# Kernel tuning notes

Measured on AMD Instinct MI355X. Metric: run time of the kernel, lower is better.

## Reference

```python
import jax, jax.numpy as jnp
import numpy as np

N = 10000        # num nodes
E = 160000       # num edges
C = 128          # hidden_channels
SCALE = 0.0625   # scale_factor = 1/avg_degree
EPS = 1.1920929e-07  # torch RMSNorm default eps = finfo(float32).eps


def setup_inputs() -> dict:
    key = jax.random.key(0)
    ks = jax.random.split(key, 10)
    s = jax.random.normal(ks[0], (N, 1, C), dtype=jnp.float32)
    v = jax.random.normal(ks[1], (N, 3, C), dtype=jnp.float32)
    edge_index = jax.random.randint(ks[2], (2, E), 0, N, dtype=jnp.int64)
    rbf_filter = jax.random.normal(ks[3], (E, 1, 3 * C), dtype=jnp.float32)
    edge_vector = jax.random.normal(ks[4], (E, 3), dtype=jnp.float32)
    # phi MLP params (Linear(C,C) -> SiLU -> Dropout(eval) -> Linear(C,3C))
    w1 = jax.random.normal(ks[5], (C, C), dtype=jnp.float32) / np.sqrt(C)
    b1 = jnp.zeros((C,), dtype=jnp.float32)
    w2 = jax.random.normal(ks[6], (3 * C, C), dtype=jnp.float32) / np.sqrt(C)
    b2 = jnp.zeros((3 * C,), dtype=jnp.float32)
    rms_w = jnp.ones((C,), dtype=jnp.float32)  # RMSNorm elementwise affine weight
    return {"s": s, "v": v, "edge_index": edge_index, "rbf_filter": rbf_filter,
            "edge_vector": edge_vector, "w1": w1, "b1": b1, "w2": w2, "b2": b2,
            "rms_w": rms_w}


def reference(s, v, edge_index, rbf_filter, edge_vector, w1, b1, w2, b2, rms_w):
    i, j = edge_index[0], edge_index[1]
    # RMSNorm over last dim
    s_norm = s * jax.lax.rsqrt(jnp.mean(s * s, axis=-1, keepdims=True) + EPS) * rms_w
    # phi MLP (dropout is identity in eval mode)
    h = jax.nn.silu(jnp.einsum('nkc,dc->nkd', s_norm, w1) + b1)
    phi_s = jnp.einsum('nkc,dc->nkd', h, w2) + b2          # [N,1,3C]
    filt = phi_s[j] * rbf_filter                           # [E,1,3C]
    m_s, m_vv, m_vs = jnp.split(filt, 3, axis=-1)          # each [E,1,C]
    ds = jax.ops.segment_sum(m_s, i, num_segments=N)       # [N,1,C]
    gate = v[j] * m_vv + edge_vector[:, :, None] * m_vs    # [E,3,C]
    dv = jax.ops.segment_sum(gate, i, num_segments=N)      # [N,3,C]
    s_out = s + ds * SCALE
    v_out = v + dv * SCALE
    return s_out, v_out
```

## Files before the change

kernel.cpp:

```cpp
#include <hip/hip_runtime.h>
#include <hip/hip_fp16.h>
#include <math.h>

#define NN 10000
#define NE 160000
#define CH 128
#define SCALE_F 0.0625f
#define EPS_F 1.1920929e-07f

__device__ __forceinline__ unsigned short f2bf(float x) {
    unsigned int u = __float_as_uint(x);
    u += 0x7FFFu + ((u >> 16) & 1u);
    return (unsigned short)(u >> 16);
}
__device__ __forceinline__ unsigned int pack2bf(float a, float b) {
    return (unsigned int)f2bf(a) | ((unsigned int)f2bf(b) << 16);
}
__device__ __forceinline__ float bf_lo(unsigned int u) { return __uint_as_float(u << 16); }
__device__ __forceinline__ float bf_hi(unsigned int u) { return __uint_as_float(u & 0xFFFF0000u); }
__device__ __forceinline__ float4 bfq(uint2 u) {
    return make_float4(bf_lo(u.x), bf_hi(u.x), bf_lo(u.y), bf_hi(u.y));
}

__global__ __launch_bounds__(256) void detect_zero_kernel(const int* __restrict__ ei,
                                                          int* __restrict__ flag,
                                                          int* __restrict__ counts) {
    int t = blockIdx.x * 256 + threadIdx.x;
    if (t < NN) counts[t] = 0;
    if (blockIdx.x == 0 && threadIdx.x < 64) {
        int val = ei[2 * threadIdx.x + 1];
        unsigned long long b = __ballot(val != 0);
        if (threadIdx.x == 0) *flag = (b == 0ULL) ? 1 : 0;
    }
}

__global__ __launch_bounds__(256) void count_kernel(const int* __restrict__ ei,
                                                    const int* __restrict__ flag,
                                                    int* __restrict__ counts) {
    int e = blockIdx.x * 256 + threadIdx.x;
    if (e >= NE) return;
    int i = (*flag) ? ei[2 * (size_t)e] : ei[e];
    atomicAdd(&counts[i], 1);
}

__global__ __launch_bounds__(1024) void scan_kernel(const int* __restrict__ counts,
                                                    int* __restrict__ offsets,
                                                    int* __restrict__ cursor) {
    __shared__ int sm[1024];
    const int t = threadIdx.x;
    const int base = t * 10;
    int vals[10];
    int lsum = 0;
    #pragma unroll
    for (int k = 0; k < 10; ++k) {
        int idx = base + k;
        int v = (idx < NN) ? counts[idx] : 0;
        vals[k] = v;
        lsum += v;
    }
    sm[t] = lsum;
    __syncthreads();
    #pragma unroll
    for (int off = 1; off < 1024; off <<= 1) {
        int add = (t >= off) ? sm[t - off] : 0;
        __syncthreads();
        sm[t] += add;
        __syncthreads();
    }
    int run = sm[t] - lsum;
    #pragma unroll
    for (int k = 0; k < 10; ++k) {
        int idx = base + k;
        if (idx < NN) { offsets[idx] = run; cursor[idx] = run; }
        run += vals[k];
    }
}

__global__ __launch_bounds__(256) void bucket_kernel(const int* __restrict__ ei,
                                                     const int* __restrict__ flag,
                                                     const float* __restrict__ ev,
                                                     int* __restrict__ cursor,
                                                     int4* __restrict__ bucket) {
    int e = blockIdx.x * 256 + threadIdx.x;
    if (e >= NE) return;
    int i, j;
    if (*flag) {
        i = ei[2 * (size_t)e];
        j = ei[2 * ((size_t)NE + e)];
    } else {
        i = ei[e];
        j = ei[NE + e];
    }
    float e0 = ev[(size_t)e * 3 + 0];
    float e1 = ev[(size_t)e * 3 + 1];
    float e2 = ev[(size_t)e * 3 + 2];
    __half2 h01 = __floats2half2_rn(e0, e1);
    __half  h2v = __float2half_rn(e2);
    unsigned int u01 = *reinterpret_cast<unsigned int*>(&h01);
    unsigned int u2  = (unsigned int)(*reinterpret_cast<unsigned short*>(&h2v));
    int pos = atomicAdd(&cursor[i], 1);
    bucket[pos] = make_int4(e, j, (int)u01, (int)u2);
}

__global__ __launch_bounds__(256) void phi_kernel(const float* __restrict__ s,
                                                  const float* __restrict__ v,
                                                  const float* __restrict__ w1,
                                                  const float* __restrict__ b1,
                                                  const float* __restrict__ w2,
                                                  const float* __restrict__ b2,
                                                  const float* __restrict__ rms_w,
                                                  unsigned int* __restrict__ rec) {
    __shared__ float sn[8][132];
    __shared__ float hh[8][132];

    const int t = threadIdx.x;
    const int n0 = blockIdx.x * 8;

    {
        const int m = t >> 5;
        const int l = t & 31;
        const int n = n0 + m;
        const float2* vsrc = (const float2*)(v + (size_t)n * 384);
        unsigned int* vdst = rec + (size_t)n * 384 + 192;
        #pragma unroll
        for (int k = 0; k < 6; ++k) {
            float2 a = vsrc[k * 32 + l];
            vdst[k * 32 + l] = pack2bf(a.x, a.y);
        }
    }

    {
        const int m = t >> 5;
        const int l = t & 31;
        const int n = n0 + m;
        float4 sv = ((const float4*)(s + (size_t)n * CH))[l];
        float ss = sv.x * sv.x + sv.y * sv.y + sv.z * sv.z + sv.w * sv.w;
        #pragma unroll
        for (int off = 16; off > 0; off >>= 1) ss += __shfl_xor(ss, off, 32);
        const float sc = rsqrtf(ss * (1.0f / CH) + EPS_F);
        float4 rw = ((const float4*)rms_w)[l];
        float4* dst = (float4*)&sn[m][l * 4];
        float4 o;
        o.x = sv.x * sc * rw.x;
        o.y = sv.y * sc * rw.y;
        o.z = sv.z * sc * rw.z;
        o.w = sv.w * sc * rw.w;
        *dst = o;
    }
    __syncthreads();

    const int d  = t & 127;
    const int mh = (t >> 7) * 4;

    {
        float acc0, acc1, acc2, acc3;
        const float bb = b1[d];
        acc0 = acc1 = acc2 = acc3 = bb;
        const float4* w1v = (const float4*)(w1 + (size_t)d * CH);
        #pragma unroll 4
        for (int kc = 0; kc < 32; ++kc) {
            float4 w = w1v[kc];
            float4 s0 = *(const float4*)&sn[mh + 0][kc * 4];
            float4 s1 = *(const float4*)&sn[mh + 1][kc * 4];
            float4 s2 = *(const float4*)&sn[mh + 2][kc * 4];
            float4 s3 = *(const float4*)&sn[mh + 3][kc * 4];
            acc0 += w.x * s0.x + w.y * s0.y + w.z * s0.z + w.w * s0.w;
            acc1 += w.x * s1.x + w.y * s1.y + w.z * s1.z + w.w * s1.w;
            acc2 += w.x * s2.x + w.y * s2.y + w.z * s2.z + w.w * s2.w;
            acc3 += w.x * s3.x + w.y * s3.y + w.z * s3.z + w.w * s3.w;
        }
        hh[mh + 0][d] = acc0 / (1.0f + __expf(-acc0));
        hh[mh + 1][d] = acc1 / (1.0f + __expf(-acc1));
        hh[mh + 2][d] = acc2 / (1.0f + __expf(-acc2));
        hh[mh + 3][d] = acc3 / (1.0f + __expf(-acc3));
    }
    __syncthreads();

    {
        float a[3][4];
        #pragma unroll
        for (int q = 0; q < 3; ++q) {
            float bb = b2[q * 128 + d];
            a[q][0] = a[q][1] = a[q][2] = a[q][3] = bb;
        }
        const float4* w2v0 = (const float4*)(w2 + (size_t)(0 * 128 + d) * CH);
        const float4* w2v1 = (const float4*)(w2 + (size_t)(1 * 128 + d) * CH);
        const float4* w2v2 = (const float4*)(w2 + (size_t)(2 * 128 + d) * CH);
        #pragma unroll 2
        for (int kc = 0; kc < 32; ++kc) {
            float4 h0 = *(const float4*)&hh[mh + 0][kc * 4];
            float4 h1 = *(const float4*)&hh[mh + 1][kc * 4];
            float4 h2 = *(const float4*)&hh[mh + 2][kc * 4];
            float4 h3 = *(const float4*)&hh[mh + 3][kc * 4];
            float4 w0 = w2v0[kc];
            float4 w1r = w2v1[kc];
            float4 w2r = w2v2[kc];
            a[0][0] += w0.x * h0.x + w0.y * h0.y + w0.z * h0.z + w0.w * h0.w;
            a[0][1] += w0.x * h1.x + w0.y * h1.y + w0.z * h1.z + w0.w * h1.w;
            a[0][2] += w0.x * h2.x + w0.y * h2.y + w0.z * h2.z + w0.w * h2.w;
            a[0][3] += w0.x * h3.x + w0.y * h3.y + w0.z * h3.z + w0.w * h3.w;
            a[1][0] += w1r.x * h0.x + w1r.y * h0.y + w1r.z * h0.z + w1r.w * h0.w;
            a[1][1] += w1r.x * h1.x + w1r.y * h1.y + w1r.z * h1.z + w1r.w * h1.w;
            a[1][2] += w1r.x * h2.x + w1r.y * h2.y + w1r.z * h2.z + w1r.w * h2.w;
            a[1][3] += w1r.x * h3.x + w1r.y * h3.y + w1r.z * h3.z + w1r.w * h3.w;
            a[2][0] += w2r.x * h0.x + w2r.y * h0.y + w2r.z * h0.z + w2r.w * h0.w;
            a[2][1] += w2r.x * h1.x + w2r.y * h1.y + w2r.z * h1.z + w2r.w * h1.w;
            a[2][2] += w2r.x * h2.x + w2r.y * h2.y + w2r.z * h2.z + w2r.w * h2.w;
            a[2][3] += w2r.x * h3.x + w2r.y * h3.y + w2r.z * h3.z + w2r.w * h3.w;
        }
        #pragma unroll
        for (int mm = 0; mm < 4; ++mm) {
            unsigned short* p = (unsigned short*)(rec + (size_t)(n0 + mh + mm) * 384);
            p[0 * 128 + d] = f2bf(a[0][mm]);
            p[1 * 128 + d] = f2bf(a[1][mm]);
            p[2 * 128 + d] = f2bf(a[2][mm]);
        }
    }
}

__global__ __launch_bounds__(256) void gather_kernel(const float* __restrict__ s,
                                                     const float* __restrict__ v,
                                                     const unsigned int* __restrict__ rec,
                                                     const float* __restrict__ rbf,
                                                     const int* __restrict__ offsets,
                                                     const int* __restrict__ counts,
                                                     const int4* __restrict__ bucket,
                                                     float* __restrict__ out_s,
                                                     float* __restrict__ out_v) {
    const int t = threadIdx.x;
    const int n = blockIdx.x * 4 + (t >> 6);
    const int l = t & 63;
    const int half = l >> 5;
    const int q = l & 31;

    float4 acc_s = make_float4(0.f, 0.f, 0.f, 0.f);
    float4 av0 = acc_s, av1 = acc_s, av2 = acc_s;

    const int beg = offsets[n];
    const int deg = counts[n];
    const int npair = deg >> 1;
    const int4* bk = bucket + beg;

    int4 ent = make_int4(0, 0, 0, 0);
    if (npair > 0) ent = bk[half];

    for (int p = 0; p < npair; ++p) {
        int4 entn = ent;
        if (p + 1 < npair) entn = bk[2 * (p + 1) + half];

        const unsigned int* rj = rec + (size_t)ent.y * 384;
        const float*        rb = rbf + (size_t)ent.x * 384;

        uint2 uS  = ((const uint2*)(rj +   0))[q];
        uint2 uVV = ((const uint2*)(rj +  64))[q];
        uint2 uVS = ((const uint2*)(rj + 128))[q];
        uint2 uV0 = ((const uint2*)(rj + 192))[q];
        uint2 uV1 = ((const uint2*)(rj + 256))[q];
        uint2 uV2 = ((const uint2*)(rj + 320))[q];
        float4 rS  = ((const float4*)(rb +   0))[q];
        float4 rVV = ((const float4*)(rb + 128))[q];
        float4 rVS = ((const float4*)(rb + 256))[q];

        __half2 h01 = *reinterpret_cast<const __half2*>(&ent.z);
        float2 ev01 = __half22float2(h01);
        unsigned short h2u = (unsigned short)(ent.w & 0xFFFF);
        float ev2 = __half2float(*reinterpret_cast<const __half*>(&h2u));

        float4 ps = bfq(uS);
        acc_s.x = fmaf(ps.x, rS.x, acc_s.x);
        acc_s.y = fmaf(ps.y, rS.y, acc_s.y);
        acc_s.z = fmaf(ps.z, rS.z, acc_s.z);
        acc_s.w = fmaf(ps.w, rS.w, acc_s.w);

        float4 pv = bfq(uVV);
        float4 pw = bfq(uVS);
        float4 mvv = make_float4(pv.x * rVV.x, pv.y * rVV.y, pv.z * rVV.z, pv.w * rVV.w);
        float4 mvs = make_float4(pw.x * rVS.x, pw.y * rVS.y, pw.z * rVS.z, pw.w * rVS.w);

        float4 v0 = bfq(uV0), v1 = bfq(uV1), v2 = bfq(uV2);
        av0.x = fmaf(v0.x, mvv.x, fmaf(ev01.x, mvs.x, av0.x));
        av0.y = fmaf(v0.y, mvv.y, fmaf(ev01.x, mvs.y, av0.y));
        av0.z = fmaf(v0.z, mvv.z, fmaf(ev01.x, mvs.z, av0.z));
        av0.w = fmaf(v0.w, mvv.w, fmaf(ev01.x, mvs.w, av0.w));
        av1.x = fmaf(v1.x, mvv.x, fmaf(ev01.y, mvs.x, av1.x));
        av1.y = fmaf(v1.y, mvv.y, fmaf(ev01.y, mvs.y, av1.y));
        av1.z = fmaf(v1.z, mvv.z, fmaf(ev01.y, mvs.z, av1.z));
        av1.w = fmaf(v1.w, mvv.w, fmaf(ev01.y, mvs.w, av1.w));
        av2.x = fmaf(v2.x, mvv.x, fmaf(ev2, mvs.x, av2.x));
        av2.y = fmaf(v2.y, mvv.y, fmaf(ev2, mvs.y, av2.y));
        av2.z = fmaf(v2.z, mvv.z, fmaf(ev2, mvs.z, av2.z));
        av2.w = fmaf(v2.w, mvv.w, fmaf(ev2, mvs.w, av2.w));

        ent = entn;
    }

    if ((deg & 1) && half == 0) {
        int4 te = bk[deg - 1];
        const unsigned int* rj = rec + (size_t)te.y * 384;
        const float*        rb = rbf + (size_t)te.x * 384;

        uint2 uS  = ((const uint2*)(rj +   0))[q];
        uint2 uVV = ((const uint2*)(rj +  64))[q];
        uint2 uVS = ((const uint2*)(rj + 128))[q];
        uint2 uV0 = ((const uint2*)(rj + 192))[q];
        uint2 uV1 = ((const uint2*)(rj + 256))[q];
        uint2 uV2 = ((const uint2*)(rj + 320))[q];
        float4 rS  = ((const float4*)(rb +   0))[q];
        float4 rVV = ((const float4*)(rb + 128))[q];
        float4 rVS = ((const float4*)(rb + 256))[q];

        __half2 h01 = *reinterpret_cast<const __half2*>(&te.z);
        float2 ev01 = __half22float2(h01);
        unsigned short h2u = (unsigned short)(te.w & 0xFFFF);
        float ev2 = __half2float(*reinterpret_cast<const __half*>(&h2u));

        float4 ps = bfq(uS);
        acc_s.x = fmaf(ps.x, rS.x, acc_s.x);
        acc_s.y = fmaf(ps.y, rS.y, acc_s.y);
        acc_s.z = fmaf(ps.z, rS.z, acc_s.z);
        acc_s.w = fmaf(ps.w, rS.w, acc_s.w);

        float4 pv = bfq(uVV);
        float4 pw = bfq(uVS);
        float4 mvv = make_float4(pv.x * rVV.x, pv.y * rVV.y, pv.z * rVV.z, pv.w * rVV.w);
        float4 mvs = make_float4(pw.x * rVS.x, pw.y * rVS.y, pw.z * rVS.z, pw.w * rVS.w);

        float4 v0 = bfq(uV0), v1 = bfq(uV1), v2 = bfq(uV2);
        av0.x = fmaf(v0.x, mvv.x, fmaf(ev01.x, mvs.x, av0.x));
        av0.y = fmaf(v0.y, mvv.y, fmaf(ev01.x, mvs.y, av0.y));
        av0.z = fmaf(v0.z, mvv.z, fmaf(ev01.x, mvs.z, av0.z));
        av0.w = fmaf(v0.w, mvv.w, fmaf(ev01.x, mvs.w, av0.w));
        av1.x = fmaf(v1.x, mvv.x, fmaf(ev01.y, mvs.x, av1.x));
        av1.y = fmaf(v1.y, mvv.y, fmaf(ev01.y, mvs.y, av1.y));
        av1.z = fmaf(v1.z, mvv.z, fmaf(ev01.y, mvs.z, av1.z));
        av1.w = fmaf(v1.w, mvv.w, fmaf(ev01.y, mvs.w, av1.w));
        av2.x = fmaf(v2.x, mvv.x, fmaf(ev2, mvs.x, av2.x));
        av2.y = fmaf(v2.y, mvv.y, fmaf(ev2, mvs.y, av2.y));
        av2.z = fmaf(v2.z, mvv.z, fmaf(ev2, mvs.z, av2.z));
        av2.w = fmaf(v2.w, mvv.w, fmaf(ev2, mvs.w, av2.w));
    }

    acc_s.x += __shfl_xor(acc_s.x, 32);
    acc_s.y += __shfl_xor(acc_s.y, 32);
    acc_s.z += __shfl_xor(acc_s.z, 32);
    acc_s.w += __shfl_xor(acc_s.w, 32);
    av0.x += __shfl_xor(av0.x, 32);
    av0.y += __shfl_xor(av0.y, 32);
    av0.z += __shfl_xor(av0.z, 32);
    av0.w += __shfl_xor(av0.w, 32);
    av1.x += __shfl_xor(av1.x, 32);
    av1.y += __shfl_xor(av1.y, 32);
    av1.z += __shfl_xor(av1.z, 32);
    av1.w += __shfl_xor(av1.w, 32);
    av2.x += __shfl_xor(av2.x, 32);
    av2.y += __shfl_xor(av2.y, 32);
    av2.z += __shfl_xor(av2.z, 32);
    av2.w += __shfl_xor(av2.w, 32);

    const size_t nb = (size_t)n;
    if (half == 0) {
        float4 sv = ((const float4*)(s + nb * CH))[q];
        ((float4*)(out_s + nb * CH))[q] =
            make_float4(sv.x + SCALE_F * acc_s.x, sv.y + SCALE_F * acc_s.y,
                        sv.z + SCALE_F * acc_s.z, sv.w + SCALE_F * acc_s.w);
        float4 w0 = ((const float4*)(v + nb * 384))[q];
        ((float4*)(out_v + nb * 384))[q] =
            make_float4(w0.x + SCALE_F * av0.x, w0.y + SCALE_F * av0.y,
                        w0.z + SCALE_F * av0.z, w0.w + SCALE_F * av0.w);
    } else {
        float4 w1 = ((const float4*)(v + nb * 384 + 128))[q];
        ((float4*)(out_v + nb * 384 + 128))[q] =
            make_float4(w1.x + SCALE_F * av1.x, w1.y + SCALE_F * av1.y,
                        w1.z + SCALE_F * av1.z, w1.w + SCALE_F * av1.w);
        float4 w2 = ((const float4*)(v + nb * 384 + 256))[q];
        ((float4*)(out_v + nb * 384 + 256))[q] =
            make_float4(w2.x + SCALE_F * av2.x, w2.y + SCALE_F * av2.y,
                        w2.z + SCALE_F * av2.z, w2.w + SCALE_F * av2.w);
    }
}

extern "C" void kernel_launch(void* const* d_in, const int* in_sizes, int n_in,
                              void* d_out, int out_size, void* d_ws, size_t ws_size,
                              hipStream_t stream) {
    const float* s    = (const float*)d_in[0];
    const float* v    = (const float*)d_in[1];
    const int*   ei   = (const int*)d_in[2];
    const float* rbf  = (const float*)d_in[3];
    const float* ev   = (const float*)d_in[4];
    const float* w1   = (const float*)d_in[5];
    const float* b1   = (const float*)d_in[6];
    const float* w2   = (const float*)d_in[7];
    const float* b2   = (const float*)d_in[8];
    const float* rmsw = (const float*)d_in[9];

    float* out   = (float*)d_out;
    float* out_s = out;
    float* out_v = out + (size_t)NN * CH;

    char* ws = (char*)d_ws;
    unsigned int* rec = (unsigned int*)ws;     ws += (size_t)NN * 384 * sizeof(unsigned int);
    int* i64flag = (int*)ws;                   ws += 64;
    int* counts  = (int*)ws;                   ws += (size_t)NN * sizeof(int);
    int* offsets = (int*)ws;                   ws += (size_t)NN * sizeof(int);
    int* cursor  = (int*)ws;                   ws += (size_t)NN * sizeof(int);
    int4* bucket = (int4*)ws;

    detect_zero_kernel<<<(NN + 255) / 256, 256, 0, stream>>>(ei, i64flag, counts);
    count_kernel<<<(NE + 255) / 256, 256, 0, stream>>>(ei, i64flag, counts);
    scan_kernel<<<1, 1024, 0, stream>>>(counts, offsets, cursor);
    bucket_kernel<<<(NE + 255) / 256, 256, 0, stream>>>(ei, i64flag, ev, cursor, bucket);
    phi_kernel<<<NN / 8, 256, 0, stream>>>(s, v, w1, b1, w2, b2, rmsw, rec);
    gather_kernel<<<NN / 4, 256, 0, stream>>>(s, v, rec, rbf, offsets, counts, bucket,
                                              out_s, out_v);
}
```

Baseline: 495.9 us.

## Transpose MLP weights and restructure phi kernel for coalesced weight reuse

```diff
diff --git a/kernel.cpp b/kernel.cpp
--- a/kernel.cpp
+++ b/kernel.cpp
@@ -31,6 +31,21 @@
         int val = ei[2 * threadIdx.x + 1];
         unsigned long long b = __ballot(val != 0);
         if (threadIdx.x == 0) *flag = (b == 0ULL) ? 1 : 0;
+    }
+}
+
+__global__ __launch_bounds__(256) void transpose_w_kernel(const float* __restrict__ w1,
+                                                          const float* __restrict__ w2,
+                                                          float* __restrict__ w1t,
+                                                          float* __restrict__ w2t) {
+    int idx = blockIdx.x * 256 + threadIdx.x;
+    if (idx < 128 * 128) {
+        int c = idx >> 7, d = idx & 127;
+        w1t[c * 128 + d] = w1[d * 128 + c];
+    } else {
+        int o = idx - 128 * 128;
+        int c = o / 384, d = o - c * 384;
+        w2t[c * 384 + d] = w2[d * 128 + c];
     }
 }
 
@@ -102,118 +117,132 @@
     bucket[pos] = make_int4(e, j, (int)u01, (int)u2);
 }
 
-__global__ __launch_bounds__(256) void phi_kernel(const float* __restrict__ s,
+__global__ __launch_bounds__(128) void phi_kernel(const float* __restrict__ s,
                                                   const float* __restrict__ v,
-                                                  const float* __restrict__ w1,
+                                                  const float* __restrict__ w1t,
                                                   const float* __restrict__ b1,
-                                                  const float* __restrict__ w2,
+                                                  const float* __restrict__ w2t,
                                                   const float* __restrict__ b2,
                                                   const float* __restrict__ rms_w,
                                                   unsigned int* __restrict__ rec) {
-    __shared__ float sn[8][132];
-    __shared__ float hh[8][132];
+    __shared__ float xw[2][8][128];
+    __shared__ float hh[2][8][128];
 
     const int t = threadIdx.x;
-    const int n0 = blockIdx.x * 8;
+    const int wv = t >> 6;
+    const int l = t & 63;
+    const int half = l >> 5;
+    const int q = l & 31;
+    const int nbase = blockIdx.x * 16 + wv * 8;
+
+    #pragma unroll
+    for (int n = 0; n < 8; ++n) {
+        const int gn = nbase + n;
+        const float2* vsrc = (const float2*)(v + (size_t)gn * 384);
+        unsigned int* vdst = rec + (size_t)gn * 384 + 192;
+        #pragma unroll
+        for (int k = 0; k < 3; ++k) {
+            float2 a = vsrc[k * 64 + l];
+            vdst[k * 64 + l] = pack2bf(a.x, a.y);
+        }
+    }
 
     {
-        const int m = t >> 5;
-        const int l = t & 31;
-        const int n = n0 + m;
-        const float2* vsrc = (const float2*)(v + (size_t)n * 384);
-        unsigned int* vdst = rec + (size_t)n * 384 + 192;
-        #pragma unroll
-        for (int k = 0; k < 6; ++k) {
-            float2 a = vsrc[k * 32 + l];
-            vdst[k * 32 + l] = pack2bf(a.x, a.y);
-        }
-    }
+        const float4 rw = ((const float4*)rms_w)[q];
+        #pragma unroll
+        for (int r = 0; r < 4; ++r) {
+            const int n = half * 4 + r;
+            const int gn = nbase + n;
+            float4 sv = ((const float4*)(s + (size_t)gn * CH))[q];
+            float ss = sv.x * sv.x + sv.y * sv.y + sv.z * sv.z + sv.w * sv.w;
+            #pragma unroll
+            for (int off = 16; off > 0; off >>= 1) ss += __shfl_xor(ss, off, 32);
+            const float sc = rsqrtf(ss * (1.0f / CH) + EPS_F);
+            float4 o;
+            o.x = sv.x * sc * rw.x;
+            o.y = sv.y * sc * rw.y;
+            o.z = sv.z * sc * rw.z;
+            o.w = sv.w * sc * rw.w;
+            *(float4*)&xw[wv][n][q * 4] = o;
+        }
+    }
+    __syncthreads();
 
     {
-        const int m = t >> 5;
-        const int l = t & 31;
-        const int n = n0 + m;
-        float4 sv = ((const float4*)(s + (size_t)n * CH))[l];
-        float ss = sv.x * sv.x + sv.y * sv.y + sv.z * sv.z + sv.w * sv.w;
-        #pragma unroll
-        for (int off = 16; off > 0; off >>= 1) ss += __shfl_xor(ss, off, 32);
-        const float sc = rsqrtf(ss * (1.0f / CH) + EPS_F);
-        float4 rw = ((const float4*)rms_w)[l];
-        float4* dst = (float4*)&sn[m][l * 4];
-        float4 o;
-        o.x = sv.x * sc * rw.x;
-        o.y = sv.y * sc * rw.y;
-        o.z = sv.z * sc * rw.z;
-        o.w = sv.w * sc * rw.w;
-        *dst = o;
+        float4 acc[8];
+        const float4 bia = ((const float4*)b1)[q];
+        #pragma unroll
+        for (int n = 0; n < 8; ++n)
+            acc[n] = (half == 0) ? bia : make_float4(0.f, 0.f, 0.f, 0.f);
+
+        #pragma unroll 4
+        for (int it = 0; it < 64; ++it) {
+            const int c = 2 * it + half;
+            const float4 w = *(const float4*)(w1t + (size_t)c * 128 + 4 * q);
+            #pragma unroll
+            for (int n = 0; n < 8; ++n) {
+                const float xv = xw[wv][n][c];
+                acc[n].x = fmaf(xv, w.x, acc[n].x);
+                acc[n].y = fmaf(xv, w.y, acc[n].y);
+                acc[n].z = fmaf(xv, w.z, acc[n].z);
+                acc[n].w = fmaf(xv, w.w, acc[n].w);
+            }
+        }
+        #pragma unroll
+        for (int n = 0; n < 8; ++n) {
+            acc[n].x += __shfl_xor(acc[n].x, 32);
+            acc[n].y += __shfl_xor(acc[n].y, 32);
+            acc[n].z += __shfl_xor(acc[n].z, 32);
+            acc[n].w += __shfl_xor(acc[n].w, 32);
+        }
+        #pragma unroll
+        for (int r = 0; r < 4; ++r) {
+            const int n = half * 4 + r;
+            float4 a = acc[n];
+            a.x = a.x / (1.0f + __expf(-a.x));
+            a.y = a.y / (1.0f + __expf(-a.y));
+            a.z = a.z / (1.0f + __expf(-a.z));
+            a.w = a.w / (1.0f + __expf(-a.w));
+            *(float4*)&hh[wv][n][q * 4] = a;
+        }
     }
     __syncthreads();
 
-    const int d  = t & 127;
-    const int mh = (t >> 7) * 4;
-
-    {
-        float acc0, acc1, acc2, acc3;
-        const float bb = b1[d];
-        acc0 = acc1 = acc2 = acc3 = bb;
-        const float4* w1v = (const float4*)(w1 + (size_t)d * CH);
+    #pragma unroll 1
+    for (int sg = 0; sg < 3; ++sg) {
+        float4 acc[8];
+        const float4 bia = ((const float4*)(b2 + 128 * sg))[q];
+        #pragma unroll
+        for (int n = 0; n < 8; ++n)
+            acc[n] = (half == 0) ? bia : make_float4(0.f, 0.f, 0.f, 0.f);
+
         #pragma unroll 4
-        for (int kc = 0; kc < 32; ++kc) {
-            float4 w = w1v[kc];
-            float4 s0 = *(const float4*)&sn[mh + 0][kc * 4];
-            float4 s1 = *(const float4*)&sn[mh + 1][kc * 4];
-            float4 s2 = *(const float4*)&sn[mh + 2][kc * 4];
-            float4 s3 = *(const float4*)&sn[mh + 3][kc * 4];
-            acc0 += w.x * s0.x + w.y * s0.y + w.z * s0.z + w.w * s0.w;
-            acc1 += w.x * s1.x + w.y * s1.y + w.z * s1.z + w.w * s1.w;
-            acc2 += w.x * s2.x + w.y * s2.y + w.z * s2.z + w.w * s2.w;
-            acc3 += w.x * s3.x + w.y * s3.y + w.z * s3.z + w.w * s3.w;
-        }
-        hh[mh + 0][d] = acc0 / (1.0f + __expf(-acc0));
-        hh[mh + 1][d] = acc1 / (1.0f + __expf(-acc1));
-        hh[mh + 2][d] = acc2 / (1.0f + __expf(-acc2));
-        hh[mh + 3][d] = acc3 / (1.0f + __expf(-acc3));
-    }
-    __syncthreads();
-
-    {
-        float a[3][4];
-        #pragma unroll
-        for (int q = 0; q < 3; ++q) {
-            float bb = b2[q * 128 + d];
-            a[q][0] = a[q][1] = a[q][2] = a[q][3] = bb;
-        }
-        const float4* w2v0 = (const float4*)(w2 + (size_t)(0 * 128 + d) * CH);
-        const float4* w2v1 = (const float4*)(w2 + (size_t)(1 * 128 + d) * CH);
-        const float4* w2v2 = (const float4*)(w2 + (size_t)(2 * 128 + d) * CH);
-        #pragma unroll 2
-        for (int kc = 0; kc < 32; ++kc) {
-            float4 h0 = *(const float4*)&hh[mh + 0][kc * 4];
-            float4 h1 = *(const float4*)&hh[mh + 1][kc * 4];
-            float4 h2 = *(const float4*)&hh[mh + 2][kc * 4];
-            float4 h3 = *(const float4*)&hh[mh + 3][kc * 4];
-            float4 w0 = w2v0[kc];
-            float4 w1r = w2v1[kc];
-            float4 w2r = w2v2[kc];
-            a[0][0] += w0.x * h0.x + w0.y * h0.y + w0.z * h0.z + w0.w * h0.w;
-            a[0][1] += w0.x * h1.x + w0.y * h1.y + w0.z * h1.z + w0.w * h1.w;
-            a[0][2] += w0.x * h2.x + w0.y * h2.y + w0.z * h2.z + w0.w * h2.w;
-            a[0][3] += w0.x * h3.x + w0.y * h3.y + w0.z * h3.z + w0.w * h3.w;
-            a[1][0] += w1r.x * h0.x + w1r.y * h0.y + w1r.z * h0.z + w1r.w * h0.w;
-            a[1][1] += w1r.x * h1.x + w1r.y * h1.y + w1r.z * h1.z + w1r.w * h1.w;
-            a[1][2] += w1r.x * h2.x + w1r.y * h2.y + w1r.z * h2.z + w1r.w * h2.w;
-            a[1][3] += w1r.x * h3.x + w1r.y * h3.y + w1r.z * h3.z + w1r.w * h3.w;
-            a[2][0] += w2r.x * h0.x + w2r.y * h0.y + w2r.z * h0.z + w2r.w * h0.w;
-            a[2][1] += w2r.x * h1.x + w2r.y * h1.y + w2r.z * h1.z + w2r.w * h1.w;
-            a[2][2] += w2r.x * h2.x + w2r.y * h2.y + w2r.z * h2.z + w2r.w * h2.w;
-            a[2][3] += w2r.x * h3.x + w2r.y * h3.y + w2r.z * h3.z + w2r.w * h3.w;
-        }
-        #pragma unroll
-        for (int mm = 0; mm < 4; ++mm) {
-            unsigned short* p = (unsigned short*)(rec + (size_t)(n0 + mh + mm) * 384);
-            p[0 * 128 + d] = f2bf(a[0][mm]);
-            p[1 * 128 + d] = f2bf(a[1][mm]);
-            p[2 * 128 + d] = f2bf(a[2][mm]);
+        for (int it = 0; it < 64; ++it) {
+            const int c = 2 * it + half;
+            const float4 w = *(const float4*)(w2t + (size_t)c * 384 + 128 * sg + 4 * q);
+            #pragma unroll
+            for (int n = 0; n < 8; ++n) {
+                const float hv = hh[wv][n][c];
+                acc[n].x = fmaf(hv, w.x, acc[n].x);
+                acc[n].y = fmaf(hv, w.y, acc[n].y);
+                acc[n].z = fmaf(hv, w.z, acc[n].z);
+                acc[n].w = fmaf(hv, w.w, acc[n].w);
+            }
+        }
+        #pragma unroll
+        for (int n = 0; n < 8; ++n) {
+            acc[n].x += __shfl_xor(acc[n].x, 32);
+            acc[n].y += __shfl_xor(acc[n].y, 32);
+            acc[n].z += __shfl_xor(acc[n].z, 32);
+            acc[n].w += __shfl_xor(acc[n].w, 32);
+        }
+        #pragma unroll
+        for (int r = 0; r < 4; ++r) {
+            const int n = half * 4 + r;
+            uint2 pk;
+            pk.x = pack2bf(acc[n].x, acc[n].y);
+            pk.y = pack2bf(acc[n].z, acc[n].w);
+            *(uint2*)(rec + (size_t)(nbase + n) * 384 + 64 * sg + 2 * q) = pk;
         }
     }
 }
@@ -402,14 +431,17 @@
     int* i64flag = (int*)ws;                   ws += 64;
     int* counts  = (int*)ws;                   ws += (size_t)NN * sizeof(int);
     int* offsets = (int*)ws;                   ws += (size_t)NN * sizeof(int);
-    int* cursor  = (int*)ws;                   ws += (size_t)NN * sizeof(int);
-    int4* bucket = (int4*)ws;
+    int* cursor  = (int*)ws;                   ws += (size_t)NN * sizeof(int) + 48;
+    int4* bucket = (int4*)ws;                  ws += (size_t)NE * sizeof(int4);
+    float* w1t   = (float*)ws;                 ws += (size_t)128 * 128 * sizeof(float);
+    float* w2t   = (float*)ws;
 
     detect_zero_kernel<<<(NN + 255) / 256, 256, 0, stream>>>(ei, i64flag, counts);
+    transpose_w_kernel<<<256, 256, 0, stream>>>(w1, w2, w1t, w2t);
     count_kernel<<<(NE + 255) / 256, 256, 0, stream>>>(ei, i64flag, counts);
     scan_kernel<<<1, 1024, 0, stream>>>(counts, offsets, cursor);
     bucket_kernel<<<(NE + 255) / 256, 256, 0, stream>>>(ei, i64flag, ev, cursor, bucket);
-    phi_kernel<<<NN / 8, 256, 0, stream>>>(s, v, w1, b1, w2, b2, rmsw, rec);
+    phi_kernel<<<NN / 16, 128, 0, stream>>>(s, v, w1t, b1, w2t, b2, rmsw, rec);
     gather_kernel<<<NN / 4, 256, 0, stream>>>(s, v, rec, rbf, offsets, counts, bucket,
                                               out_s, out_v);
 }
```

New measurement: 463.2 us. -6.6%, faster.
